# Kernel tuning notes

Hardware: AMD Instinct MI355X
Metric: run time of the kernel (lower is better)

## Reference

```python
import jax, jax.numpy as jnp
import numpy as np

ALPHA = 0.2      # LeakyReLU negative slope
NEG = -9e15      # mask value from the original code


def setup_inputs() -> dict:
    key = jax.random.key(0)
    k1, k2, k3, k4 = jax.random.split(key, 4)
    N, F_in, F_out = 8192, 128, 64
    x = jax.random.normal(k1, (N, F_in), dtype=jnp.float32)
    adj = jax.random.randint(k2, (N, N), 0, 2).astype(jnp.float32)
    # xavier_uniform with gain=1.414
    gain = 1.414
    limW = gain * np.sqrt(6.0 / (F_in + F_out))
    W = jax.random.uniform(k3, (F_in, F_out), minval=-limW, maxval=limW, dtype=jnp.float32)
    lima = gain * np.sqrt(6.0 / (2 * F_out + 1))
    a = jax.random.uniform(k4, (2 * F_out, 1), minval=-lima, maxval=lima, dtype=jnp.float32)
    return {"x": x, "adj": adj, "W": W, "a": a}


def reference(x, adj, W, a):
    # h: [N, F_out]
    h = x @ W
    F_out = W.shape[1]
    # Additive score decomposes: e[i,j] = leakyrelu(a1.h_i + a2.h_j)
    # (exact same math as the repeat/cat construction, without the N*N*2F tensor)
    s1 = h @ a[:F_out, 0]   # [N]
    s2 = h @ a[F_out:, 0]   # [N]
    pre = s1[:, None] + s2[None, :]                      # [N, N]
    e = jnp.where(pre >= 0, pre, ALPHA * pre)            # LeakyReLU
    # Original: attention = where(adj > 0, adj * e, -9e15) then row softmax
    attention = jnp.where(adj > 0, adj * e, NEG)
    attention = jax.nn.softmax(attention, axis=1)
    # (dropout skipped: inference mode, training=False)
    h_prime = attention @ h                              # [N, F_out]
    return jax.nn.elu(h_prime)                           # concat=True -> ELU
```

## Files before the change

### kernel.cpp

```cpp
#include <hip/hip_runtime.h>
#include <math.h>

#define N 8192
#define FIN 128
#define FOUT 64
#define ALPHA 0.2f
#define JS 16
#define JLEN (N / JS)
#define NT (JLEN / 32)

typedef __attribute__((ext_vector_type(8))) short bf16x8;
typedef __attribute__((ext_vector_type(8))) unsigned short ushort8;
typedef __attribute__((ext_vector_type(4))) float f32x4;
typedef __attribute__((ext_vector_type(4))) int i32x4;

__device__ __forceinline__ unsigned f2bf(float f) {
    unsigned int u = __float_as_uint(f);
    u += 0x7fff + ((u >> 16) & 1);
    return u >> 16;
}
__device__ __forceinline__ float elu(float v) { return v > 0.f ? v : expm1f(v); }
__device__ __forceinline__ float lrelu(float p) { return fmaxf(p, ALPHA * p); }

__device__ __forceinline__ void gll16(const void* src, void* dst_lds) {
    __builtin_amdgcn_global_load_lds((const __attribute__((address_space(1))) void*)src,
                                     (__attribute__((address_space(3))) void*)dst_lds, 16, 0, 0);
}

__global__ __launch_bounds__(256) void k_h(const float* __restrict__ x,
                                           const float* __restrict__ W,
                                           const float* __restrict__ a,
                                           float* __restrict__ h,
                                           float* __restrict__ s1,
                                           float* __restrict__ s2) {
    __shared__ float Wl[FIN * FOUT];
    int t = threadIdx.x;
    #pragma unroll
    for (int i = 0; i < (FIN * FOUT) / (256 * 4); ++i) {
        int idx = (t + i * 256) * 4;
        *(float4*)&Wl[idx] = *(const float4*)&W[idx];
    }
    __syncthreads();
    int gid = blockIdx.x * 256 + t;
    int row = gid >> 6;
    int c   = gid & 63;
    float acc = 0.f;
    #pragma unroll
    for (int k = 0; k < FIN; k += 4) {
        float4 xv = *(const float4*)&x[row * FIN + k];
        acc = fmaf(xv.x, Wl[(k + 0) * FOUT + c], acc);
        acc = fmaf(xv.y, Wl[(k + 1) * FOUT + c], acc);
        acc = fmaf(xv.z, Wl[(k + 2) * FOUT + c], acc);
        acc = fmaf(xv.w, Wl[(k + 3) * FOUT + c], acc);
    }
    h[gid] = acc;
    float p1 = acc * a[c];
    float p2 = acc * a[64 + c];
    #pragma unroll
    for (int off = 32; off; off >>= 1) {
        p1 += __shfl_xor(p1, off);
        p2 += __shfl_xor(p2, off);
    }
    if (c == 0) { s1[row] = p1; s2[row] = p2; }
}

__global__ __launch_bounds__(256) void k_max(const float* __restrict__ s2,
                                             float* __restrict__ s2max) {
    __shared__ float red[256];
    float m = -1e30f;
    for (int i = threadIdx.x; i < N; i += 256) m = fmaxf(m, s2[i]);
    red[threadIdx.x] = m;
    __syncthreads();
    #pragma unroll
    for (int s = 128; s; s >>= 1) {
        if (threadIdx.x < s) red[threadIdx.x] = fmaxf(red[threadIdx.x], red[threadIdx.x + s]);
        __syncthreads();
    }
    if (threadIdx.x == 0) *s2max = red[0];
}

__global__ __launch_bounds__(256) void k_t(const float* __restrict__ h,
                                           const float* __restrict__ s2,
                                           unsigned short* __restrict__ hT,
                                           float* __restrict__ e2p_g,
                                           float* __restrict__ e2n_g) {
    __shared__ float tile[64][65];
    int t = threadIdx.x;
    int j0 = blockIdx.x * 64;
    #pragma unroll
    for (int p = 0; p < 4; ++p) {
        int j = p * 16 + (t >> 4);
        int c4 = (t & 15) * 4;
        float4 v = *(const float4*)&h[(size_t)(j0 + j) * 64 + c4];
        tile[j][c4] = v.x; tile[j][c4 + 1] = v.y; tile[j][c4 + 2] = v.z; tile[j][c4 + 3] = v.w;
    }
    __syncthreads();
    int c = t & 63, seg = t >> 6;
    ushort8 u0, u1;
    #pragma unroll
    for (int k = 0; k < 8; ++k) u0[k] = (unsigned short)f2bf(tile[seg * 16 + k][c]);
    #pragma unroll
    for (int k = 0; k < 8; ++k) u1[k] = (unsigned short)f2bf(tile[seg * 16 + 8 + k][c]);
    unsigned short* dst = &hT[(size_t)c * N + j0 + seg * 16];
    *(ushort8*)dst = u0;
    *(ushort8*)(dst + 8) = u1;
    if (t < 64) {
        int j = j0 + t;
        float s = s2[j];
        e2p_g[j] = __expf(s);
        e2n_g[j] = __expf(ALPHA * s);
    }
}

__global__ __launch_bounds__(256, 4) void k_attn(const float* __restrict__ adj,
                                                 const unsigned short* __restrict__ hT,
                                                 const float* __restrict__ s1,
                                                 const float* __restrict__ s2max,
                                                 const float* __restrict__ e2p_g,
                                                 const float* __restrict__ e2n_g,
                                                 float* __restrict__ pacc,
                                                 float* __restrict__ pden) {
    __shared__ __align__(16) char hbuf[2][4096];
    __shared__ float e2p_l[JLEN];
    __shared__ float e2n_l[JLEN];

    int tid  = threadIdx.x;
    int wave = tid >> 6;
    int lane = tid & 63;
    int rb   = blockIdx.x / JS;
    int js   = blockIdx.x % JS;
    int r0   = rb * 64;
    int jb   = js * JLEN;

    int row = lane & 15;
    int kg  = lane >> 4;
    int kg8 = kg * 8;
    int r   = r0 + wave * 16 + row;

    int ldsrow = tid >> 2;
    int cslot  = tid & 3;
    int gchunk = (cslot - (ldsrow >> 1)) & 3;
    const unsigned short* hsrc = hT + (size_t)ldsrow * N + jb + gchunk * 8;
    char* ldst0 = &hbuf[0][tid * 16];
    char* ldst1 = &hbuf[1][tid * 16];

    gll16(hsrc, ldst0);
    {
        int t2 = tid * 2;
        *(float2*)&e2p_l[t2] = *(const float2*)&e2p_g[jb + t2];
        *(float2*)&e2n_l[t2] = *(const float2*)&e2n_g[jb + t2];
    }
    float s1v = s1[r];
    float S2M = *s2max;
    float Mv  = lrelu(s1v + S2M);
    float E1p = __expf(s1v - Mv);
    float E1n = __expf(ALPHA * s1v - Mv);
    float expC = __expf(-s1v);

    asm volatile("s_waitcnt vmcnt(0)" ::: "memory");
    __syncthreads();

    f32x4 acc0 = {0.f, 0.f, 0.f, 0.f};
    f32x4 acc1 = {0.f, 0.f, 0.f, 0.f};
    f32x4 acc2 = {0.f, 0.f, 0.f, 0.f};
    f32x4 acc3 = {0.f, 0.f, 0.f, 0.f};
    float den = 0.f;

    const size_t rbase = (size_t)r * N + jb;
    int bbyte = row * 64 + (((kg + (row >> 1)) & 3) * 16);

    #pragma unroll 2
    for (int t = 0; t < NT; ++t) {
        if (t + 1 < NT)
            gll16(hsrc + (t + 1) * 32, ((t + 1) & 1) ? ldst1 : ldst0);

        int jj = t * 32 + kg8;
        float4 a0 = *(const float4*)&adj[rbase + jj];
        float4 a1 = *(const float4*)&adj[rbase + jj + 4];
        float4 p0 = *(const float4*)&e2p_l[jj];
        float4 p1 = *(const float4*)&e2p_l[jj + 4];
        float4 n0 = *(const float4*)&e2n_l[jj];
        float4 n1 = *(const float4*)&e2n_l[jj + 4];

        float w0 = a0.x * ((p0.x >= expC) ? p0.x * E1p : n0.x * E1n);
        float w1 = a0.y * ((p0.y >= expC) ? p0.y * E1p : n0.y * E1n);
        float w2 = a0.z * ((p0.z >= expC) ? p0.z * E1p : n0.z * E1n);
        float w3 = a0.w * ((p0.w >= expC) ? p0.w * E1p : n0.w * E1n);
        float w4 = a1.x * ((p1.x >= expC) ? p1.x * E1p : n1.x * E1n);
        float w5 = a1.y * ((p1.y >= expC) ? p1.y * E1p : n1.y * E1n);
        float w6 = a1.z * ((p1.z >= expC) ? p1.z * E1p : n1.z * E1n);
        float w7 = a1.w * ((p1.w >= expC) ? p1.w * E1p : n1.w * E1n);
        den += w0 + w1 + w2 + w3 + w4 + w5 + w6 + w7;

        i32x4 pk;
        pk[0] = (int)(f2bf(w0) | (f2bf(w1) << 16));
        pk[1] = (int)(f2bf(w2) | (f2bf(w3) << 16));
        pk[2] = (int)(f2bf(w4) | (f2bf(w5) << 16));
        pk[3] = (int)(f2bf(w6) | (f2bf(w7) << 16));
        bf16x8 af = __builtin_bit_cast(bf16x8, pk);

        const char* bb = (t & 1) ? &hbuf[1][0] : &hbuf[0][0];
        bf16x8 b0 = *(const bf16x8*)(bb + bbyte);
        bf16x8 b1 = *(const bf16x8*)(bb + bbyte + 1024);
        bf16x8 b2 = *(const bf16x8*)(bb + bbyte + 2048);
        bf16x8 b3 = *(const bf16x8*)(bb + bbyte + 3072);
        acc0 = __builtin_amdgcn_mfma_f32_16x16x32_bf16(af, b0, acc0, 0, 0, 0);
        acc1 = __builtin_amdgcn_mfma_f32_16x16x32_bf16(af, b1, acc1, 0, 0, 0);
        acc2 = __builtin_amdgcn_mfma_f32_16x16x32_bf16(af, b2, acc2, 0, 0, 0);
        acc3 = __builtin_amdgcn_mfma_f32_16x16x32_bf16(af, b3, acc3, 0, 0, 0);

        asm volatile("s_waitcnt vmcnt(0)" ::: "memory");
        __syncthreads();
    }

    den += __shfl_xor(den, 16);
    den += __shfl_xor(den, 32);

    int r0w = r0 + wave * 16;
    #pragma unroll
    for (int q = 0; q < 4; ++q) {
        int ro = kg * 4 + q;
        size_t ob = ((size_t)js * N + r0w + ro) * 64 + row;
        pacc[ob + 0]  = acc0[q];
        pacc[ob + 16] = acc1[q];
        pacc[ob + 32] = acc2[q];
        pacc[ob + 48] = acc3[q];
    }
    if (lane < 16) pden[(size_t)js * N + r0w + lane] = den;
}

__global__ __launch_bounds__(256) void k_combine(const float* __restrict__ pacc,
                                                 const float* __restrict__ pden,
                                                 float* __restrict__ out) {
    int gid = blockIdx.x * 256 + threadIdx.x;
    int row = gid >> 6;
    float a = 0.f, d = 0.f;
    #pragma unroll
    for (int s = 0; s < JS; ++s) {
        a += pacc[((size_t)s * N + row) * 64 + (gid & 63)];
        d += pden[(size_t)s * N + row];
    }
    out[gid] = elu(a / d);
}

extern "C" void kernel_launch(void* const* d_in, const int* in_sizes, int n_in,
                              void* d_out, int out_size, void* d_ws, size_t ws_size,
                              hipStream_t stream) {
    const float* x   = (const float*)d_in[0];
    const float* adj = (const float*)d_in[1];
    const float* W   = (const float*)d_in[2];
    const float* a   = (const float*)d_in[3];
    float* out = (float*)d_out;

    float* ws    = (float*)d_ws;
    float* h     = ws;
    float* s1    = h + (size_t)N * FOUT;
    float* s2    = s1 + N;
    float* s2m   = s2 + N;
    float* e2p_g = s2m + 64;
    float* e2n_g = e2p_g + N;
    float* pden  = e2n_g + N;
    unsigned short* hT = (unsigned short*)(pden + JS * N);
    float* pacc  = (float*)hT + 262144;

    k_h<<<dim3((N * FOUT) / 256), dim3(256), 0, stream>>>(x, W, a, h, s1, s2);
    k_max<<<dim3(1), dim3(256), 0, stream>>>(s2, s2m);
    k_t<<<dim3(N / 64), dim3(256), 0, stream>>>(h, s2, hT, e2p_g, e2n_g);

    k_attn<<<dim3(128 * JS), dim3(256), 0, stream>>>(adj, hT, s1, s2m, e2p_g, e2n_g, pacc, pden);
    k_combine<<<dim3((N * FOUT) / 256), dim3(256), 0, stream>>>(pacc, pden, out);
}
```

Before: 102.8 us.

## Deepen attention pipeline with register-prefetched adj and 4-buffer LDS, fuse max via atomics

Replaces the single-block max-reduction kernel with an order-preserving atomicMax in the h kernel, removing one launch. The attention kernel now prefetches the next adjacency tile into registers and keeps two h tiles in flight in a 4-slot LDS ring. It waits on a partial vmcnt with a bare s_barrier instead of draining all loads each iteration. JS halves from 16 to 8, so each block covers a longer j range and fewer partials go to the combine step, at the cost of fewer blocks and more LDS per block.

New measurement: 177.1 us. 72.2% more time.

```diff
diff --git a/kernel.cpp b/kernel.cpp
--- a/kernel.cpp
+++ b/kernel.cpp
@@ -5,7 +5,7 @@
 #define FIN 128
 #define FOUT 64
 #define ALPHA 0.2f
-#define JS 16
+#define JS 8
 #define JLEN (N / JS)
 #define NT (JLEN / 32)
 
@@ -21,6 +21,10 @@
 }
 __device__ __forceinline__ float elu(float v) { return v > 0.f ? v : expm1f(v); }
 __device__ __forceinline__ float lrelu(float p) { return fmaxf(p, ALPHA * p); }
+__device__ __forceinline__ unsigned fenc(float f) {
+    unsigned u = __float_as_uint(f);
+    return (u & 0x80000000u) ? ~u : (u | 0x80000000u);
+}
 
 __device__ __forceinline__ void gll16(const void* src, void* dst_lds) {
     __builtin_amdgcn_global_load_lds((const __attribute__((address_space(1))) void*)src,
@@ -32,7 +36,8 @@
                                            const float* __restrict__ a,
                                            float* __restrict__ h,
                                            float* __restrict__ s1,
-                                           float* __restrict__ s2) {
+                                           float* __restrict__ s2,
+                                           unsigned* __restrict__ s2me) {
     __shared__ float Wl[FIN * FOUT];
     int t = threadIdx.x;
     #pragma unroll
@@ -61,22 +66,11 @@
         p1 += __shfl_xor(p1, off);
         p2 += __shfl_xor(p2, off);
     }
-    if (c == 0) { s1[row] = p1; s2[row] = p2; }
-}
-
-__global__ __launch_bounds__(256) void k_max(const float* __restrict__ s2,
-                                             float* __restrict__ s2max) {
-    __shared__ float red[256];
-    float m = -1e30f;
-    for (int i = threadIdx.x; i < N; i += 256) m = fmaxf(m, s2[i]);
-    red[threadIdx.x] = m;
-    __syncthreads();
-    #pragma unroll
-    for (int s = 128; s; s >>= 1) {
-        if (threadIdx.x < s) red[threadIdx.x] = fmaxf(red[threadIdx.x], red[threadIdx.x + s]);
-        __syncthreads();
-    }
-    if (threadIdx.x == 0) *s2max = red[0];
+    if (c == 0) {
+        s1[row] = p1;
+        s2[row] = p2;
+        atomicMax(s2me, fenc(p2));
+    }
 }
 
 __global__ __launch_bounds__(256) void k_t(const float* __restrict__ h,
@@ -115,12 +109,12 @@
 __global__ __launch_bounds__(256, 4) void k_attn(const float* __restrict__ adj,
                                                  const unsigned short* __restrict__ hT,
                                                  const float* __restrict__ s1,
-                                                 const float* __restrict__ s2max,
+                                                 const unsigned* __restrict__ s2me,
                                                  const float* __restrict__ e2p_g,
                                                  const float* __restrict__ e2n_g,
                                                  float* __restrict__ pacc,
                                                  float* __restrict__ pden) {
-    __shared__ __align__(16) char hbuf[2][4096];
+    __shared__ __align__(16) char hbuf[4][4096];
     __shared__ float e2p_l[JLEN];
     __shared__ float e2n_l[JLEN];
 
@@ -141,24 +135,27 @@
     int cslot  = tid & 3;
     int gchunk = (cslot - (ldsrow >> 1)) & 3;
     const unsigned short* hsrc = hT + (size_t)ldsrow * N + jb + gchunk * 8;
-    char* ldst0 = &hbuf[0][tid * 16];
-    char* ldst1 = &hbuf[1][tid * 16];
-
-    gll16(hsrc, ldst0);
+
+    gll16(hsrc, &hbuf[0][tid * 16]);
+    const size_t rbase = (size_t)r * N + jb;
+    float4 A0 = *(const float4*)&adj[rbase + kg8];
+    float4 A1 = *(const float4*)&adj[rbase + kg8 + 4];
+    float4 B0, B1;
+    gll16(hsrc + 32, &hbuf[1][tid * 16]);
     {
-        int t2 = tid * 2;
-        *(float2*)&e2p_l[t2] = *(const float2*)&e2p_g[jb + t2];
-        *(float2*)&e2n_l[t2] = *(const float2*)&e2n_g[jb + t2];
+        int t4 = tid * 4;
+        *(float4*)&e2p_l[t4] = *(const float4*)&e2p_g[jb + t4];
+        *(float4*)&e2n_l[t4] = *(const float4*)&e2n_g[jb + t4];
     }
     float s1v = s1[r];
-    float S2M = *s2max;
+    unsigned em = *s2me;
+    float S2M = __uint_as_float((em & 0x80000000u) ? (em & 0x7fffffffu) : ~em);
     float Mv  = lrelu(s1v + S2M);
     float E1p = __expf(s1v - Mv);
     float E1n = __expf(ALPHA * s1v - Mv);
     float expC = __expf(-s1v);
 
-    asm volatile("s_waitcnt vmcnt(0)" ::: "memory");
-    __syncthreads();
+    asm volatile("s_waitcnt lgkmcnt(0)" ::: "memory");
 
     f32x4 acc0 = {0.f, 0.f, 0.f, 0.f};
     f32x4 acc1 = {0.f, 0.f, 0.f, 0.f};
@@ -166,52 +163,57 @@
     f32x4 acc3 = {0.f, 0.f, 0.f, 0.f};
     float den = 0.f;
 
-    const size_t rbase = (size_t)r * N + jb;
     int bbyte = row * 64 + (((kg + (row >> 1)) & 3) * 16);
 
-    #pragma unroll 2
-    for (int t = 0; t < NT; ++t) {
-        if (t + 1 < NT)
-            gll16(hsrc + (t + 1) * 32, ((t + 1) & 1) ? ldst1 : ldst0);
-
-        int jj = t * 32 + kg8;
-        float4 a0 = *(const float4*)&adj[rbase + jj];
-        float4 a1 = *(const float4*)&adj[rbase + jj + 4];
-        float4 p0 = *(const float4*)&e2p_l[jj];
-        float4 p1 = *(const float4*)&e2p_l[jj + 4];
-        float4 n0 = *(const float4*)&e2n_l[jj];
-        float4 n1 = *(const float4*)&e2n_l[jj + 4];
-
-        float w0 = a0.x * ((p0.x >= expC) ? p0.x * E1p : n0.x * E1n);
-        float w1 = a0.y * ((p0.y >= expC) ? p0.y * E1p : n0.y * E1n);
-        float w2 = a0.z * ((p0.z >= expC) ? p0.z * E1p : n0.z * E1n);
-        float w3 = a0.w * ((p0.w >= expC) ? p0.w * E1p : n0.w * E1n);
-        float w4 = a1.x * ((p1.x >= expC) ? p1.x * E1p : n1.x * E1n);
-        float w5 = a1.y * ((p1.y >= expC) ? p1.y * E1p : n1.y * E1n);
-        float w6 = a1.z * ((p1.z >= expC) ? p1.z * E1p : n1.z * E1n);
-        float w7 = a1.w * ((p1.w >= expC) ? p1.w * E1p : n1.w * E1n);
-        den += w0 + w1 + w2 + w3 + w4 + w5 + w6 + w7;
-
-        i32x4 pk;
-        pk[0] = (int)(f2bf(w0) | (f2bf(w1) << 16));
-        pk[1] = (int)(f2bf(w2) | (f2bf(w3) << 16));
-        pk[2] = (int)(f2bf(w4) | (f2bf(w5) << 16));
-        pk[3] = (int)(f2bf(w6) | (f2bf(w7) << 16));
-        bf16x8 af = __builtin_bit_cast(bf16x8, pk);
-
-        const char* bb = (t & 1) ? &hbuf[1][0] : &hbuf[0][0];
-        bf16x8 b0 = *(const bf16x8*)(bb + bbyte);
-        bf16x8 b1 = *(const bf16x8*)(bb + bbyte + 1024);
-        bf16x8 b2 = *(const bf16x8*)(bb + bbyte + 2048);
-        bf16x8 b3 = *(const bf16x8*)(bb + bbyte + 3072);
-        acc0 = __builtin_amdgcn_mfma_f32_16x16x32_bf16(af, b0, acc0, 0, 0, 0);
-        acc1 = __builtin_amdgcn_mfma_f32_16x16x32_bf16(af, b1, acc1, 0, 0, 0);
-        acc2 = __builtin_amdgcn_mfma_f32_16x16x32_bf16(af, b2, acc2, 0, 0, 0);
-        acc3 = __builtin_amdgcn_mfma_f32_16x16x32_bf16(af, b3, acc3, 0, 0, 0);
-
-        asm volatile("s_waitcnt vmcnt(0)" ::: "memory");
-        __syncthreads();
-    }
+#define BODY(u, C0, C1, N0, N1) do {                                           \
+        int t  = 4 * p + (u);                                                  \
+        int tn = (t + 1 < NT) ? t + 1 : NT - 1;                                \
+        int ts = (t + 2 < NT) ? t + 2 : NT - 1;                                \
+        N0 = *(const float4*)&adj[rbase + tn * 32 + kg8];                      \
+        N1 = *(const float4*)&adj[rbase + tn * 32 + kg8 + 4];                  \
+        gll16(hsrc + ts * 32, &hbuf[((u) + 2) & 3][tid * 16]);                 \
+        asm volatile("s_waitcnt vmcnt(4)" ::: "memory");                       \
+        __builtin_amdgcn_sched_barrier(0);                                     \
+        __builtin_amdgcn_s_barrier();                                          \
+        __builtin_amdgcn_sched_barrier(0);                                     \
+        int jj = t * 32 + kg8;                                                 \
+        float4 p0 = *(const float4*)&e2p_l[jj];                                \
+        float4 p1 = *(const float4*)&e2p_l[jj + 4];                            \
+        float4 n0 = *(const float4*)&e2n_l[jj];                                \
+        float4 n1 = *(const float4*)&e2n_l[jj + 4];                            \
+        float w0 = C0.x * ((p0.x >= expC) ? p0.x * E1p : n0.x * E1n);          \
+        float w1 = C0.y * ((p0.y >= expC) ? p0.y * E1p : n0.y * E1n);          \
+        float w2 = C0.z * ((p0.z >= expC) ? p0.z * E1p : n0.z * E1n);          \
+        float w3 = C0.w * ((p0.w >= expC) ? p0.w * E1p : n0.w * E1n);          \
+        float w4 = C1.x * ((p1.x >= expC) ? p1.x * E1p : n1.x * E1n);          \
+        float w5 = C1.y * ((p1.y >= expC) ? p1.y * E1p : n1.y * E1n);          \
+        float w6 = C1.z * ((p1.z >= expC) ? p1.z * E1p : n1.z * E1n);          \
+        float w7 = C1.w * ((p1.w >= expC) ? p1.w * E1p : n1.w * E1n);          \
+        den += w0 + w1 + w2 + w3 + w4 + w5 + w6 + w7;                          \
+        i32x4 pk;                                                              \
+        pk[0] = (int)(f2bf(w0) | (f2bf(w1) << 16));                            \
+        pk[1] = (int)(f2bf(w2) | (f2bf(w3) << 16));                            \
+        pk[2] = (int)(f2bf(w4) | (f2bf(w5) << 16));                            \
+        pk[3] = (int)(f2bf(w6) | (f2bf(w7) << 16));                            \
+        bf16x8 af = __builtin_bit_cast(bf16x8, pk);                            \
+        const char* bb = &hbuf[(u) & 3][0];                                    \
+        bf16x8 b0 = *(const bf16x8*)(bb + bbyte);                              \
+        bf16x8 b1 = *(const bf16x8*)(bb + bbyte + 1024);                       \
+        bf16x8 b2 = *(const bf16x8*)(bb + bbyte + 2048);                       \
+        bf16x8 b3 = *(const bf16x8*)(bb + bbyte + 3072);                       \
+        acc0 = __builtin_amdgcn_mfma_f32_16x16x32_bf16(af, b0, acc0, 0, 0, 0); \
+        acc1 = __builtin_amdgcn_mfma_f32_16x16x32_bf16(af, b1, acc1, 0, 0, 0); \
+        acc2 = __builtin_amdgcn_mfma_f32_16x16x32_bf16(af, b2, acc2, 0, 0, 0); \
+        acc3 = __builtin_amdgcn_mfma_f32_16x16x32_bf16(af, b3, acc3, 0, 0, 0); \
+    } while (0)
+
+    for (int p = 0; p < NT / 4; ++p) {
+        BODY(0, A0, A1, B0, B1);
+        BODY(1, B0, B1, A0, A1);
+        BODY(2, A0, A1, B0, B1);
+        BODY(3, B0, B1, A0, A1);
+    }
+#undef BODY
 
     den += __shfl_xor(den, 16);
     den += __shfl_xor(den, 32);
@@ -256,17 +258,17 @@
     float* h     = ws;
     float* s1    = h + (size_t)N * FOUT;
     float* s2    = s1 + N;
-    float* s2m   = s2 + N;
-    float* e2p_g = s2m + 64;
+    unsigned* s2me = (unsigned*)(s2 + N);
+    float* e2p_g = (float*)s2me + 64;
     float* e2n_g = e2p_g + N;
     float* pden  = e2n_g + N;
     unsigned short* hT = (unsigned short*)(pden + JS * N);
     float* pacc  = (float*)hT + 262144;
 
-    k_h<<<dim3((N * FOUT) / 256), dim3(256), 0, stream>>>(x, W, a, h, s1, s2);
-    k_max<<<dim3(1), dim3(256), 0, stream>>>(s2, s2m);
+    hipMemsetAsync(s2me, 0, sizeof(unsigned), stream);
+    k_h<<<dim3((N * FOUT) / 256), dim3(256), 0, stream>>>(x, W, a, h, s1, s2, s2me);
     k_t<<<dim3(N / 64), dim3(256), 0, stream>>>(h, s2, hT, e2p_g, e2n_g);
 
-    k_attn<<<dim3(128 * JS), dim3(256), 0, stream>>>(adj, hT, s1, s2m, e2p_g, e2n_g, pacc, pden);
+    k_attn<<<dim3(128 * JS), dim3(256), 0, stream>>>(adj, hT, s1, s2me, e2p_g, e2n_g, pacc, pden);
     k_combine<<<dim3((N * FOUT) / 256), dim3(256), 0, stream>>>(pacc, pden, out);
 }
```

## Fuse s2 max and exp precompute into k_h via atomicMax, halve j-splits

Applied to the files above, without the earlier changes.

Removes the single-block k_max reduction kernel by having k_h compute the global max of s2 with an atomicMax on an order-preserving unsigned encoding, and moves the exp(s2) precompute from k_t into k_h. This drops one serial launch and a single-block reduction from the critical path, at the cost of a memset and contention on one atomic. It also halves the number of column splits (JS 16 to 8), so each attention block covers more columns, loads float4 of exp values, and the partial-sum buffers and combine work shrink, with fewer blocks for occupancy.

New measurement: 180.0 us. 1.75x slower.

```diff
diff --git a/kernel.cpp b/kernel.cpp
--- a/kernel.cpp
+++ b/kernel.cpp
@@ -5,7 +5,7 @@
 #define FIN 128
 #define FOUT 64
 #define ALPHA 0.2f
-#define JS 16
+#define JS 8
 #define JLEN (N / JS)
 #define NT (JLEN / 32)
 
@@ -21,6 +21,10 @@
 }
 __device__ __forceinline__ float elu(float v) { return v > 0.f ? v : expm1f(v); }
 __device__ __forceinline__ float lrelu(float p) { return fmaxf(p, ALPHA * p); }
+__device__ __forceinline__ unsigned fenc(float f) {
+    unsigned u = __float_as_uint(f);
+    return (u & 0x80000000u) ? ~u : (u | 0x80000000u);
+}
 
 __device__ __forceinline__ void gll16(const void* src, void* dst_lds) {
     __builtin_amdgcn_global_load_lds((const __attribute__((address_space(1))) void*)src,
@@ -32,7 +36,10 @@
                                            const float* __restrict__ a,
                                            float* __restrict__ h,
                                            float* __restrict__ s1,
-                                           float* __restrict__ s2) {
+                                           float* __restrict__ s2,
+                                           unsigned* __restrict__ s2me,
+                                           float* __restrict__ e2p_g,
+                                           float* __restrict__ e2n_g) {
     __shared__ float Wl[FIN * FOUT];
     int t = threadIdx.x;
     #pragma unroll
@@ -61,29 +68,17 @@
         p1 += __shfl_xor(p1, off);
         p2 += __shfl_xor(p2, off);
     }
-    if (c == 0) { s1[row] = p1; s2[row] = p2; }
-}
-
-__global__ __launch_bounds__(256) void k_max(const float* __restrict__ s2,
-                                             float* __restrict__ s2max) {
-    __shared__ float red[256];
-    float m = -1e30f;
-    for (int i = threadIdx.x; i < N; i += 256) m = fmaxf(m, s2[i]);
-    red[threadIdx.x] = m;
-    __syncthreads();
-    #pragma unroll
-    for (int s = 128; s; s >>= 1) {
-        if (threadIdx.x < s) red[threadIdx.x] = fmaxf(red[threadIdx.x], red[threadIdx.x + s]);
-        __syncthreads();
-    }
-    if (threadIdx.x == 0) *s2max = red[0];
+    if (c == 0) {
+        s1[row] = p1;
+        s2[row] = p2;
+        e2p_g[row] = __expf(p2);
+        e2n_g[row] = __expf(ALPHA * p2);
+        atomicMax(s2me, fenc(p2));
+    }
 }
 
 __global__ __launch_bounds__(256) void k_t(const float* __restrict__ h,
-                                           const float* __restrict__ s2,
-                                           unsigned short* __restrict__ hT,
-                                           float* __restrict__ e2p_g,
-                                           float* __restrict__ e2n_g) {
+                                           unsigned short* __restrict__ hT) {
     __shared__ float tile[64][65];
     int t = threadIdx.x;
     int j0 = blockIdx.x * 64;
@@ -104,18 +99,12 @@
     unsigned short* dst = &hT[(size_t)c * N + j0 + seg * 16];
     *(ushort8*)dst = u0;
     *(ushort8*)(dst + 8) = u1;
-    if (t < 64) {
-        int j = j0 + t;
-        float s = s2[j];
-        e2p_g[j] = __expf(s);
-        e2n_g[j] = __expf(ALPHA * s);
-    }
 }
 
 __global__ __launch_bounds__(256, 4) void k_attn(const float* __restrict__ adj,
                                                  const unsigned short* __restrict__ hT,
                                                  const float* __restrict__ s1,
-                                                 const float* __restrict__ s2max,
+                                                 const unsigned* __restrict__ s2me,
                                                  const float* __restrict__ e2p_g,
                                                  const float* __restrict__ e2n_g,
                                                  float* __restrict__ pacc,
@@ -146,12 +135,13 @@
 
     gll16(hsrc, ldst0);
     {
-        int t2 = tid * 2;
-        *(float2*)&e2p_l[t2] = *(const float2*)&e2p_g[jb + t2];
-        *(float2*)&e2n_l[t2] = *(const float2*)&e2n_g[jb + t2];
+        int t4 = tid * 4;
+        *(float4*)&e2p_l[t4] = *(const float4*)&e2p_g[jb + t4];
+        *(float4*)&e2n_l[t4] = *(const float4*)&e2n_g[jb + t4];
     }
     float s1v = s1[r];
-    float S2M = *s2max;
+    unsigned em = *s2me;
+    float S2M = __uint_as_float((em & 0x80000000u) ? (em & 0x7fffffffu) : ~em);
     float Mv  = lrelu(s1v + S2M);
     float E1p = __expf(s1v - Mv);
     float E1n = __expf(ALPHA * s1v - Mv);
@@ -256,17 +246,17 @@
     float* h     = ws;
     float* s1    = h + (size_t)N * FOUT;
     float* s2    = s1 + N;
-    float* s2m   = s2 + N;
-    float* e2p_g = s2m + 64;
+    unsigned* s2me = (unsigned*)(s2 + N);
+    float* e2p_g = (float*)s2me + 64;
     float* e2n_g = e2p_g + N;
     float* pden  = e2n_g + N;
     unsigned short* hT = (unsigned short*)(pden + JS * N);
     float* pacc  = (float*)hT + 262144;
 
-    k_h<<<dim3((N * FOUT) / 256), dim3(256), 0, stream>>>(x, W, a, h, s1, s2);
-    k_max<<<dim3(1), dim3(256), 0, stream>>>(s2, s2m);
-    k_t<<<dim3(N / 64), dim3(256), 0, stream>>>(h, s2, hT, e2p_g, e2n_g);
-
-    k_attn<<<dim3(128 * JS), dim3(256), 0, stream>>>(adj, hT, s1, s2m, e2p_g, e2n_g, pacc, pden);
+    hipMemsetAsync(s2me, 0, sizeof(unsigned), stream);
+    k_h<<<dim3((N * FOUT) / 256), dim3(256), 0, stream>>>(x, W, a, h, s1, s2, s2me, e2p_g, e2n_g);
+    k_t<<<dim3(N / 64), dim3(256), 0, stream>>>(h, hT);
+
+    k_attn<<<dim3(128 * JS), dim3(256), 0, stream>>>(adj, hT, s1, s2me, e2p_g, e2n_g, pacc, pden);
     k_combine<<<dim3((N * FOUT) / 256), dim3(256), 0, stream>>>(pacc, pden, out);
 }
```
